# Performance work log

Measured on AMD Instinct MI355X. Metric: run time of the kernel, lower is better.

## Reference

```python
import jax, jax.numpy as jnp
import numpy as np

# Dims: B samples, D=2048 backbone feature dim (resnet50 fc.in_features),
B, D, G, R, K, C = 16384, 2048, 8, 6, 3, 16


def setup_inputs() -> dict:
    key = jax.random.key(0)
    k0, k1, k2, k3 = jax.random.split(key, 4)
    feats = jax.random.normal(k0, (B, D), dtype=jnp.float32)          # backbone output (dropout=eval identity)
    roi_ids = jax.random.randint(k1, (B,), 0, G)                       # per-sample routing id (roi_names)
    W_reg = jax.random.normal(k2, (G, R, D), dtype=jnp.float32) * 0.02  # reg_heads[roi].weight
    b_reg = jnp.zeros((G, R), dtype=jnp.float32)                       # reg_heads[roi].bias
    W_cls = jax.random.normal(k3, (G, K, C, D), dtype=jnp.float32) * 0.02  # cls_heads[roi][k].weight
    b_cls = jnp.zeros((G, K, C), dtype=jnp.float32)                    # cls_heads[roi][k].bias
    return {"feats": feats, "roi_ids": roi_ids, "W_reg": W_reg, "b_reg": b_reg,
            "W_cls": W_cls, "b_cls": b_cls}


def reference(feats, roi_ids, W_reg, b_reg, W_cls, b_cls):
    # Original loop applies, per sample i, the Linear heads of roi_names[i].
    # Vectorized: compute all-ROI head outputs densely, then gather the routed one.
    # (Same math per sample; dropout is identity in eval mode.)
    reg_all = jnp.einsum('bd,grd->bgr', feats, W_reg) + b_reg[None]        # [B, G, R]
    cls_all = jnp.einsum('bd,gkcd->bgkc', feats, W_cls) + b_cls[None]      # [B, G, K, C]
    reg = jnp.take_along_axis(reg_all, roi_ids[:, None, None], axis=1)[:, 0]            # [B, R]
    cls = jnp.take_along_axis(cls_all, roi_ids[:, None, None, None], axis=1)[:, 0]      # [B, K, C]
    return reg, cls
```

## Files before the change

### kernel.cpp

```cpp
#include <hip/hip_runtime.h>
#include <hip/hip_bf16.h>

#define NB   16384
#define NG   8
#define ND   2048
#define NR   6
#define NKC  48
#define NOUT 54
#define NT32 (NB / 32 + NG)
#define LROW 136
#define BM   32
#define KC   128
#define NCH  (ND / KC)
#define MAXT (NB / BM + NG)

typedef __attribute__((ext_vector_type(8))) short short8_t;
typedef __attribute__((ext_vector_type(4))) float f32x4;

__device__ __forceinline__ unsigned short f2bf(float x) {
    union { float f; unsigned u; } v; v.f = x;
    unsigned r = v.u + 0x7FFFu + ((v.u >> 16) & 1u);
    return (unsigned short)(r >> 16);
}

__device__ __forceinline__ short8_t cvt8(float4 a, float4 b) {
    short8_t s;
    s[0] = (short)f2bf(a.x); s[1] = (short)f2bf(a.y);
    s[2] = (short)f2bf(a.z); s[3] = (short)f2bf(a.w);
    s[4] = (short)f2bf(b.x); s[5] = (short)f2bf(b.y);
    s[6] = (short)f2bf(b.z); s[7] = (short)f2bf(b.w);
    return s;
}

__device__ __forceinline__ void gl_lds16(const void* g, void* s) {
    __builtin_amdgcn_global_load_lds(
        (const __attribute__((address_space(1))) void*)g,
        (__attribute__((address_space(3))) void*)s,
        16, 0, 0);
}

#define WAITV(N) do { asm volatile("s_waitcnt vmcnt(" #N ")" ::: "memory"); \
                      __builtin_amdgcn_sched_barrier(0); } while (0)
#define BAR() do { __builtin_amdgcn_s_barrier(); \
                   __builtin_amdgcn_sched_barrier(0); } while (0)

__global__ void hist_kernel(const int* __restrict__ roi, int* __restrict__ counts) {
    int i = blockIdx.x * 256 + threadIdx.x;
    int g = roi[i];
    int lane = threadIdx.x & 63;
    #pragma unroll
    for (int gg = 0; gg < NG; ++gg) {
        unsigned long long m = __ballot(g == gg);
        if (m && lane == (int)(__ffsll((unsigned long long)m) - 1))
            atomicAdd(&counts[gg], (int)__popcll(m));
    }
}

__global__ void scatter_kernel(const int* __restrict__ roi, const int* __restrict__ counts,
                               int* __restrict__ ranks, int* __restrict__ perm) {
    int off[NG];
    int acc = 0;
    #pragma unroll
    for (int gg = 0; gg < NG; ++gg) { off[gg] = acc; acc += counts[gg]; }
    int i = blockIdx.x * 256 + threadIdx.x;
    int g = roi[i];
    int lane = threadIdx.x & 63;
    #pragma unroll
    for (int gg = 0; gg < NG; ++gg) {
        unsigned long long m = __ballot(g == gg);
        if (!m) continue;
        int leader = (int)(__ffsll((unsigned long long)m) - 1);
        int base = 0;
        if (lane == leader) base = atomicAdd(&ranks[gg], (int)__popcll(m));
        base = __shfl(base, leader);
        if (g == gg) {
            int rank = (int)__popcll(m & ((1ull << lane) - 1ull));
            perm[off[gg] + base + rank] = i;
        }
    }
}

__global__ void prep_kernel(const int* __restrict__ roi, int* __restrict__ cnt,
                            int* __restrict__ rank,
                            const float* __restrict__ Wreg, const float* __restrict__ Wcls,
                            short* __restrict__ Wbf) {
    if (blockIdx.x < 64) {
        int i = blockIdx.x * 256 + threadIdx.x;
        int g = roi[i];
        int lane = threadIdx.x & 63;
        #pragma unroll
        for (int gg = 0; gg < NG; ++gg) {
            unsigned long long m = __ballot(g == gg);
            if (!m) continue;
            int leader = (int)(__ffsll((unsigned long long)m) - 1);
            int base = 0;
            if (lane == leader) base = atomicAdd(&cnt[gg], (int)__popcll(m));
            base = __shfl(base, leader);
            if (g == gg) {
                int r = (int)__popcll(m & ((1ull << lane) - 1ull));
                rank[i] = base + r;
            }
        }
    } else {
        int u = (blockIdx.x - 64) * 256 + threadIdx.x;
        int l = u & 63;
        int q = (u >> 6) & 7;
        int c = (u >> 9) & 31;
        int g = u >> 14;
        int n = q >> 1, ks = q & 1;
        int row = n * 16 + (l & 15);
        int k   = c * 64 + ks * 32 + (l >> 4) * 8;
        short8_t v = {0, 0, 0, 0, 0, 0, 0, 0};
        if (row < NOUT) {
            const float* s = (row < NR) ? Wreg + (size_t)(g * NR + row) * ND + k
                                        : Wcls + (size_t)(g * NKC + row - NR) * ND + k;
            float4 a = *(const float4*)s;
            float4 b = *(const float4*)(s + 4);
            v = cvt8(a, b);
        }
        *(short8_t*)(Wbf + (size_t)u * 8) = v;
    }
}

__global__ void castgather_kernel(const float* __restrict__ feats,
                                  const int* __restrict__ roi,
                                  const int* __restrict__ cnt, const int* __restrict__ rank,
                                  short* __restrict__ gathered, int* __restrict__ permp) {
    int b = blockIdx.x;
    int tid = threadIdx.x;
    int g = roi[b];
    int pre = 0;
    #pragma unroll
    for (int gg = 0; gg < NG; ++gg) if (gg < g) pre += cnt[gg];
    int pos = pre + rank[b];
    if (tid == 0) permp[pos] = b;
    const float* src = feats + (size_t)b * ND + tid * 8;
    float4 a0 = *(const float4*)(src);
    float4 a1 = *(const float4*)(src + 4);
    *(short8_t*)(gathered + (size_t)pos * ND + tid * 8) = cvt8(a0, a1);
}

__launch_bounds__(256, 4)
__global__ void gemm_s_kernel(const short* __restrict__ gathered,
                              const short* __restrict__ Wbf,
                              const float* __restrict__ breg, const float* __restrict__ bcls,
                              const int* __restrict__ cnt, const int* __restrict__ permp,
                              float* __restrict__ out) {
    __shared__ __align__(16) char lds[3][12288];

    int tid = threadIdx.x, w = tid >> 6, l = tid & 63, lr = l & 15, lq = l >> 4;
    int mt = w >> 1, nh = w & 1;

    int ts[NG + 1]; ts[0] = 0;
    int pre[NG]; int acc_ = 0;
    #pragma unroll
    for (int gg = 0; gg < NG; ++gg) {
        pre[gg] = acc_;
        acc_ += cnt[gg];
        ts[gg + 1] = ts[gg] + ((cnt[gg] + 31) >> 5);
    }
    int b = blockIdx.x;
    if (b >= ts[NG]) return;
    int g = 0;
    #pragma unroll
    for (int gg = 0; gg < NG; ++gg) if (b >= ts[gg + 1]) g = gg + 1;
    int rbase = (b - ts[g]) * 32;
    int nv = cnt[g] - rbase; if (nv > 32) nv = 32;
    int t32 = pre[g] + rbase;

    int rr = w * 8 + (l >> 3);
    const char* aSrc = (const char*)gathered + ((size_t)t32 + rr) * 4096
                     + (((l & 7) ^ (rr & 7)) << 4);
    const char* bSrc = (const char*)Wbf + (size_t)g * 262144 + 2 * w * 1024 + l * 16;

    const int ra0 = (mt * 16 + lr) * 128 + ((((0 * 4) + lq) ^ (lr & 7)) << 4);
    const int ra1 = (mt * 16 + lr) * 128 + ((((1 * 4) + lq) ^ (lr & 7)) << 4);
    const int rb00 = 4096 + ((nh * 2 + 0) * 2 + 0) * 1024 + l * 16;
    const int rb01 = 4096 + ((nh * 2 + 0) * 2 + 1) * 1024 + l * 16;
    const int rb10 = 4096 + ((nh * 2 + 1) * 2 + 0) * 1024 + l * 16;
    const int rb11 = 4096 + ((nh * 2 + 1) * 2 + 1) * 1024 + l * 16;

#define STAGE(cc, sl) do {                                                     \
        gl_lds16(aSrc + (size_t)(cc) * 128, &lds[sl][w * 1024 + l * 16]);      \
        const char* b_ = bSrc + (size_t)(cc) * 8192;                           \
        gl_lds16(b_,        &lds[sl][4096 + 2 * w * 1024 + l * 16]);           \
        gl_lds16(b_ + 1024, &lds[sl][4096 + 2 * w * 1024 + 1024 + l * 16]);    \
    } while (0)

    f32x4 acc0 = {0, 0, 0, 0}, acc1 = {0, 0, 0, 0};

    STAGE(0, 0); STAGE(1, 1);
    int csl = 0;
    #pragma unroll
    for (int c = 0; c < 32; ++c) {
        if (c + 2 < 32) STAGE(c + 2, (c + 2) % 3);
        if (c < 30)       WAITV(6);
        else if (c == 30) WAITV(3);
        else              WAITV(0);
        BAR();
        {
            const char* s = &lds[csl][0];
            short8_t af0 = *(const short8_t*)(s + ra0);
            short8_t b00 = *(const short8_t*)(s + rb00);
            short8_t b10 = *(const short8_t*)(s + rb10);
            acc0 = __builtin_amdgcn_mfma_f32_16x16x32_bf16(af0, b00, acc0, 0, 0, 0);
            acc1 = __builtin_amdgcn_mfma_f32_16x16x32_bf16(af0, b10, acc1, 0, 0, 0);
            short8_t af1 = *(const short8_t*)(s + ra1);
            short8_t b01 = *(const short8_t*)(s + rb01);
            short8_t b11 = *(const short8_t*)(s + rb11);
            acc0 = __builtin_amdgcn_mfma_f32_16x16x32_bf16(af1, b01, acc0, 0, 0, 0);
            acc1 = __builtin_amdgcn_mfma_f32_16x16x32_bf16(af1, b11, acc1, 0, 0, 0);
        }
        BAR();
        csl = (csl == 2) ? 0 : csl + 1;
    }
#undef STAGE

    const int B6 = NB * NR;
    #pragma unroll
    for (int cn = 0; cn < 2; ++cn) {
        f32x4 v = cn ? acc1 : acc0;
        int col = nh * 32 + cn * 16 + lr;
        if (col < NOUT) {
            float bias = (col < NR) ? breg[g * NR + col] : bcls[g * NKC + (col - NR)];
            #pragma unroll
            for (int j = 0; j < 4; ++j) {
                int row = mt * 16 + lq * 4 + j;
                if (row < nv) {
                    int smp = permp[t32 + row];
                    if (col < NR) out[smp * NR + col] = v[j] + bias;
                    else          out[B6 + smp * NKC + (col - NR)] = v[j] + bias;
                }
            }
        }
    }
}

__launch_bounds__(256, 3)
__global__ void gemm_kernel(const float* __restrict__ feats,
                            const float* __restrict__ Wreg, const float* __restrict__ breg,
                            const float* __restrict__ Wcls, const float* __restrict__ bcls,
                            const int* __restrict__ counts, const int* __restrict__ perm,
                            float* __restrict__ out, int stride) {
    __shared__ __align__(16) short Bsh[2][64][LROW];
    __shared__ int sRow[BM];

    int ts[NG + 1]; ts[0] = 0;
    int off[NG]; int acc = 0;
    #pragma unroll
    for (int gg = 0; gg < NG; ++gg) {
        int c = counts[gg];
        off[gg] = stride ? gg * stride : acc;
        acc += c;
        ts[gg + 1] = ts[gg] + (c + BM - 1) / BM;
    }
    int b = blockIdx.x;
    if (b >= ts[NG]) return;
    int g = 0;
    #pragma unroll
    for (int gg = 0; gg < NG; ++gg) if (b >= ts[gg + 1]) g = gg + 1;
    int gcnt  = counts[g];
    int goff  = off[g];
    int rbase = (b - ts[g]) * BM;
    int nvalid = gcnt - rbase; if (nvalid > BM) nvalid = BM;

    int tid = threadIdx.x;
    if (tid < BM) {
        int r = rbase + tid;
        if (r >= gcnt) r = gcnt - 1;
        sRow[tid] = perm[goff + r];
    }
    __syncthreads();

    int rB = tid >> 2;
    int cq = tid & 3;
    const float* wsrc = nullptr;
    if (rB < NR)        wsrc = Wreg + ((size_t)g * NR + rB) * ND + cq * 32;
    else if (rB < NOUT) wsrc = Wcls + ((size_t)g * NKC + (rB - NR)) * ND + cq * 32;

    int w = tid >> 6, l = tid & 63, lr = l & 15, lq = l >> 4;
    int mt = w & 1, nh = w >> 1;
    const float* aptr = feats + (size_t)sRow[mt * 16 + lr] * ND + lq * 8;
    const short* brp = (const short*)&Bsh[0][0][0] + (nh * 32 + lr) * LROW + lq * 8;

    f32x4 acc0 = {0, 0, 0, 0}, acc1 = {0, 0, 0, 0};
    float4 rb[8];

    if (wsrc) {
        #pragma unroll
        for (int i = 0; i < 8; ++i) rb[i] = *(const float4*)(wsrc + 4 * i);
    } else {
        #pragma unroll
        for (int i = 0; i < 8; ++i) rb[i] = make_float4(0.f, 0.f, 0.f, 0.f);
    }
    {
        short* bw = &Bsh[0][rB][cq * 32];
        #pragma unroll
        for (int j = 0; j < 4; ++j) *(short8_t*)(bw + 8 * j) = cvt8(rb[2 * j], rb[2 * j + 1]);
    }
    __syncthreads();

    #pragma unroll
    for (int c = 0; c < NCH; ++c) {
        const int cur = c & 1, nxt = cur ^ 1;
        if (c + 1 < NCH && wsrc) {
            const float* s = wsrc + (c + 1) * KC;
            #pragma unroll
            for (int i = 0; i < 8; ++i) rb[i] = *(const float4*)(s + 4 * i);
        }
        const short* bp = brp + cur * (64 * LROW);
        const float* ap = aptr + c * KC;
        #pragma unroll
        for (int ks = 0; ks < 4; ++ks) {
            float4 a0 = *(const float4*)(ap + ks * 32);
            float4 a1 = *(const float4*)(ap + ks * 32 + 4);
            short8_t af = cvt8(a0, a1);
            short8_t b0 = *(const short8_t*)(bp + ks * 32);
            short8_t b1 = *(const short8_t*)(bp + 16 * LROW + ks * 32);
            acc0 = __builtin_amdgcn_mfma_f32_16x16x32_bf16(af, b0, acc0, 0, 0, 0);
            acc1 = __builtin_amdgcn_mfma_f32_16x16x32_bf16(af, b1, acc1, 0, 0, 0);
        }
        if (c + 1 < NCH && wsrc) {
            short* bw = &Bsh[nxt][rB][cq * 32];
            #pragma unroll
            for (int j = 0; j < 4; ++j) *(short8_t*)(bw + 8 * j) = cvt8(rb[2 * j], rb[2 * j + 1]);
        } else if (c + 1 < NCH) {
            short8_t z = {0,0,0,0,0,0,0,0};
            short* bw = &Bsh[nxt][rB][cq * 32];
            #pragma unroll
            for (int j = 0; j < 4; ++j) *(short8_t*)(bw + 8 * j) = z;
        }
        __syncthreads();
    }

    const int B6 = NB * NR;
    #pragma unroll
    for (int n = 0; n < 2; ++n) {
        f32x4 v = n ? acc1 : acc0;
        int col = nh * 32 + n * 16 + lr;
        if (col < NOUT) {
            #pragma unroll
            for (int j = 0; j < 4; ++j) {
                int row = mt * 16 + lq * 4 + j;
                if (row < nvalid) {
                    int smp = sRow[row];
                    if (col < NR) out[smp * NR + col] = v[j] + breg[g * NR + col];
                    else          out[B6 + smp * NKC + (col - NR)] = v[j] + bcls[g * NKC + (col - NR)];
                }
            }
        }
    }
}

__global__ void fallback_kernel(const float* __restrict__ feats, const int* __restrict__ roi,
                                const float* __restrict__ Wreg, const float* __restrict__ breg,
                                const float* __restrict__ Wcls, const float* __restrict__ bcls,
                                float* __restrict__ out) {
    int i = blockIdx.x;
    int lane = threadIdx.x;
    int g = roi[i];
    const float* frow = feats + (size_t)i * ND;
    float f[32];
    #pragma unroll
    for (int q = 0; q < 32; ++q) f[q] = frow[lane + 64 * q];
    for (int o = 0; o < NOUT; ++o) {
        const float* wrow = (o < NR) ? Wreg + ((size_t)g * NR + o) * ND
                                     : Wcls + ((size_t)g * NKC + (o - NR)) * ND;
        float p = 0.f;
        #pragma unroll
        for (int q = 0; q < 32; ++q) p += f[q] * wrow[lane + 64 * q];
        #pragma unroll
        for (int s = 32; s; s >>= 1) p += __shfl_xor(p, s);
        if (lane == 0) {
            if (o < NR) out[i * NR + o] = p + breg[g * NR + o];
            else        out[NB * NR + i * NKC + (o - NR)] = p + bcls[g * NKC + (o - NR)];
        }
    }
}

extern "C" void kernel_launch(void* const* d_in, const int* in_sizes, int n_in,
                              void* d_out, int out_size, void* d_ws, size_t ws_size,
                              hipStream_t stream) {
    const float* feats = (const float*)d_in[0];
    const int*   roi   = (const int*)d_in[1];
    const float* Wreg  = (const float*)d_in[2];
    const float* breg  = (const float*)d_in[3];
    const float* Wcls  = (const float*)d_in[4];
    const float* bcls  = (const float*)d_in[5];
    float* out = (float*)d_out;

    const size_t wbfBytes = (size_t)NG * 131072 * 2;
    const size_t cntOff   = 2u * 1024 * 1024;
    const size_t rankOff  = cntOff + 256;
    const size_t permOff  = rankOff + (size_t)NB * 4;
    const size_t gathOff  = 4u * 1024 * 1024;
    const size_t need_t1  = gathOff + (size_t)(NB + 32) * 4096;
    const size_t need_t3  = 256 + (size_t)NB * 4;

    if (ws_size >= need_t1) {
        short* Wbf     = (short*)d_ws;
        int*   cnt     = (int*)((char*)d_ws + cntOff);
        int*   rank    = (int*)((char*)d_ws + rankOff);
        int*   permp   = (int*)((char*)d_ws + permOff);
        short* gathered= (short*)((char*)d_ws + gathOff);
        hipMemsetAsync(cnt, 0, 64, stream);
        prep_kernel<<<576, 256, 0, stream>>>(roi, cnt, rank, Wreg, Wcls, Wbf);
        castgather_kernel<<<NB, 256, 0, stream>>>(feats, roi, cnt, rank, gathered, permp);
        gemm_s_kernel<<<NT32, 256, 0, stream>>>(gathered, Wbf, breg, bcls, cnt, permp, out);
    } else if (ws_size >= need_t3) {
        int* counts = (int*)d_ws;
        int* ranks  = counts + 8;
        int* perm   = counts + 64;
        hipMemsetAsync(counts, 0, 16 * sizeof(int), stream);
        hist_kernel<<<NB / 256, 256, 0, stream>>>(roi, counts);
        scatter_kernel<<<NB / 256, 256, 0, stream>>>(roi, counts, ranks, perm);
        gemm_kernel<<<MAXT, 256, 0, stream>>>(feats, Wreg, breg, Wcls, bcls, counts, perm, out, 0);
    } else {
        fallback_kernel<<<NB, 64, 0, stream>>>(feats, roi, Wreg, breg, Wcls, bcls, out);
    }
}
```

Baseline: 84.53 us.

## Use 128-row tiles with split-K across two blocks and atomic accumulation

The grouped GEMM now uses 512-thread blocks handling 128 rows each, with each wave computing a 32x32 output sub-tile so that loaded W tiles are reused across more rows. The K dimension is split in half across paired blocks, which combine their partial results into the output through atomicAdd, with only the first half adding the bias. This requires zeroing the output with a memset beforehand and adds atomic traffic. Padding per group grows to 128 rows, so some blocks do wasted work on small groups.

```diff
diff --git a/kernel.cpp b/kernel.cpp
--- a/kernel.cpp
+++ b/kernel.cpp
@@ -7,7 +7,6 @@
 #define NR   6
 #define NKC  48
 #define NOUT 54
-#define NT32 (NB / 32 + NG)
 #define LROW 136
 #define BM   32
 #define KC   128
@@ -140,16 +139,16 @@
     *(short8_t*)(gathered + (size_t)pos * ND + tid * 8) = cvt8(a0, a1);
 }
 
-__launch_bounds__(256, 4)
-__global__ void gemm_s_kernel(const short* __restrict__ gathered,
+__launch_bounds__(512, 2)
+__global__ void gemm_w_kernel(const short* __restrict__ gathered,
                               const short* __restrict__ Wbf,
                               const float* __restrict__ breg, const float* __restrict__ bcls,
                               const int* __restrict__ cnt, const int* __restrict__ permp,
                               float* __restrict__ out) {
-    __shared__ __align__(16) char lds[3][12288];
+    __shared__ __align__(16) char lds[3][24576];
 
     int tid = threadIdx.x, w = tid >> 6, l = tid & 63, lr = l & 15, lq = l >> 4;
-    int mt = w >> 1, nh = w & 1;
+    int rw = w >> 1, ch = w & 1;
 
     int ts[NG + 1]; ts[0] = 0;
     int pre[NG]; int acc_ = 0;
@@ -157,59 +156,73 @@
     for (int gg = 0; gg < NG; ++gg) {
         pre[gg] = acc_;
         acc_ += cnt[gg];
-        ts[gg + 1] = ts[gg] + ((cnt[gg] + 31) >> 5);
+        ts[gg + 1] = ts[gg] + ((cnt[gg] + 127) >> 7);
     }
     int b = blockIdx.x;
-    if (b >= ts[NG]) return;
+    if (b >= 2 * ts[NG]) return;
+    int t = b >> 1, kh = b & 1;
     int g = 0;
     #pragma unroll
-    for (int gg = 0; gg < NG; ++gg) if (b >= ts[gg + 1]) g = gg + 1;
-    int rbase = (b - ts[g]) * 32;
-    int nv = cnt[g] - rbase; if (nv > 32) nv = 32;
-    int t32 = pre[g] + rbase;
-
-    int rr = w * 8 + (l >> 3);
-    const char* aSrc = (const char*)gathered + ((size_t)t32 + rr) * 4096
-                     + (((l & 7) ^ (rr & 7)) << 4);
-    const char* bSrc = (const char*)Wbf + (size_t)g * 262144 + 2 * w * 1024 + l * 16;
-
-    const int ra0 = (mt * 16 + lr) * 128 + ((((0 * 4) + lq) ^ (lr & 7)) << 4);
-    const int ra1 = (mt * 16 + lr) * 128 + ((((1 * 4) + lq) ^ (lr & 7)) << 4);
-    const int rb00 = 4096 + ((nh * 2 + 0) * 2 + 0) * 1024 + l * 16;
-    const int rb01 = 4096 + ((nh * 2 + 0) * 2 + 1) * 1024 + l * 16;
-    const int rb10 = 4096 + ((nh * 2 + 1) * 2 + 0) * 1024 + l * 16;
-    const int rb11 = 4096 + ((nh * 2 + 1) * 2 + 1) * 1024 + l * 16;
+    for (int gg = 0; gg < NG; ++gg) if (t >= ts[gg + 1]) g = gg + 1;
+    int rbase = (t - ts[g]) * 128;
+    int nv = cnt[g] - rbase; if (nv > 128) nv = 128;
+    int t128 = pre[g] + rbase;
+
+    int r0 = 16 * w + (l >> 3);
+    int r1 = r0 + 8;
+    const char* a0c = (const char*)gathered + ((size_t)t128 + r0) * 4096 + kh * 2048
+                    + (((l & 7) ^ (r0 & 7)) << 4);
+    const char* a1c = (const char*)gathered + ((size_t)t128 + r1) * 4096 + kh * 2048
+                    + (((l & 7) ^ (r1 & 7)) << 4);
+    const char* bSrc = (const char*)Wbf + ((size_t)(g * 32 + kh * 16) * 8 + w) * 1024 + l * 16;
 
 #define STAGE(cc, sl) do {                                                     \
-        gl_lds16(aSrc + (size_t)(cc) * 128, &lds[sl][w * 1024 + l * 16]);      \
-        const char* b_ = bSrc + (size_t)(cc) * 8192;                           \
-        gl_lds16(b_,        &lds[sl][4096 + 2 * w * 1024 + l * 16]);           \
-        gl_lds16(b_ + 1024, &lds[sl][4096 + 2 * w * 1024 + 1024 + l * 16]);    \
+        gl_lds16(a0c + (size_t)(cc) * 128, &lds[sl][(16 * w) * 128]);          \
+        gl_lds16(a1c + (size_t)(cc) * 128, &lds[sl][(16 * w + 8) * 128]);      \
+        gl_lds16(bSrc + (size_t)(cc) * 8192, &lds[sl][16384 + w * 1024]);      \
     } while (0)
 
-    f32x4 acc0 = {0, 0, 0, 0}, acc1 = {0, 0, 0, 0};
+    const int key = lr & 7;
+    const int Rb0 = (rw * 32 + lr) * 128;
+    const int Rb1 = (rw * 32 + 16 + lr) * 128;
+    const int ra00 = Rb0 + (((0 * 4 + lq) ^ key) << 4);
+    const int ra01 = Rb0 + (((1 * 4 + lq) ^ key) << 4);
+    const int ra10 = Rb1 + (((0 * 4 + lq) ^ key) << 4);
+    const int ra11 = Rb1 + (((1 * 4 + lq) ^ key) << 4);
+    const int rb00 = 16384 + ((ch * 2 + 0) * 2 + 0) * 1024 + l * 16;
+    const int rb01 = 16384 + ((ch * 2 + 0) * 2 + 1) * 1024 + l * 16;
+    const int rb10 = 16384 + ((ch * 2 + 1) * 2 + 0) * 1024 + l * 16;
+    const int rb11 = 16384 + ((ch * 2 + 1) * 2 + 1) * 1024 + l * 16;
+
+    f32x4 acc00 = {0,0,0,0}, acc01 = {0,0,0,0}, acc10 = {0,0,0,0}, acc11 = {0,0,0,0};
 
     STAGE(0, 0); STAGE(1, 1);
     int csl = 0;
     #pragma unroll
-    for (int c = 0; c < 32; ++c) {
-        if (c + 2 < 32) STAGE(c + 2, (c + 2) % 3);
-        if (c < 30)       WAITV(6);
-        else if (c == 30) WAITV(3);
+    for (int c = 0; c < 16; ++c) {
+        if (c + 2 < 16) STAGE(c + 2, (c + 2) % 3);
+        if (c < 14)       WAITV(6);
+        else if (c == 14) WAITV(3);
         else              WAITV(0);
         BAR();
         {
             const char* s = &lds[csl][0];
-            short8_t af0 = *(const short8_t*)(s + ra0);
-            short8_t b00 = *(const short8_t*)(s + rb00);
-            short8_t b10 = *(const short8_t*)(s + rb10);
-            acc0 = __builtin_amdgcn_mfma_f32_16x16x32_bf16(af0, b00, acc0, 0, 0, 0);
-            acc1 = __builtin_amdgcn_mfma_f32_16x16x32_bf16(af0, b10, acc1, 0, 0, 0);
-            short8_t af1 = *(const short8_t*)(s + ra1);
-            short8_t b01 = *(const short8_t*)(s + rb01);
-            short8_t b11 = *(const short8_t*)(s + rb11);
-            acc0 = __builtin_amdgcn_mfma_f32_16x16x32_bf16(af1, b01, acc0, 0, 0, 0);
-            acc1 = __builtin_amdgcn_mfma_f32_16x16x32_bf16(af1, b11, acc1, 0, 0, 0);
+            short8_t af00 = *(const short8_t*)(s + ra00);
+            short8_t af10 = *(const short8_t*)(s + ra10);
+            short8_t b00  = *(const short8_t*)(s + rb00);
+            short8_t b10  = *(const short8_t*)(s + rb10);
+            acc00 = __builtin_amdgcn_mfma_f32_16x16x32_bf16(af00, b00, acc00, 0, 0, 0);
+            acc01 = __builtin_amdgcn_mfma_f32_16x16x32_bf16(af00, b10, acc01, 0, 0, 0);
+            acc10 = __builtin_amdgcn_mfma_f32_16x16x32_bf16(af10, b00, acc10, 0, 0, 0);
+            acc11 = __builtin_amdgcn_mfma_f32_16x16x32_bf16(af10, b10, acc11, 0, 0, 0);
+            short8_t af01 = *(const short8_t*)(s + ra01);
+            short8_t af11 = *(const short8_t*)(s + ra11);
+            short8_t b01  = *(const short8_t*)(s + rb01);
+            short8_t b11  = *(const short8_t*)(s + rb11);
+            acc00 = __builtin_amdgcn_mfma_f32_16x16x32_bf16(af01, b01, acc00, 0, 0, 0);
+            acc01 = __builtin_amdgcn_mfma_f32_16x16x32_bf16(af01, b11, acc01, 0, 0, 0);
+            acc10 = __builtin_amdgcn_mfma_f32_16x16x32_bf16(af11, b01, acc10, 0, 0, 0);
+            acc11 = __builtin_amdgcn_mfma_f32_16x16x32_bf16(af11, b11, acc11, 0, 0, 0);
         }
         BAR();
         csl = (csl == 2) ? 0 : csl + 1;
@@ -218,18 +231,22 @@
 
     const int B6 = NB * NR;
     #pragma unroll
-    for (int cn = 0; cn < 2; ++cn) {
-        f32x4 v = cn ? acc1 : acc0;
-        int col = nh * 32 + cn * 16 + lr;
-        if (col < NOUT) {
-            float bias = (col < NR) ? breg[g * NR + col] : bcls[g * NKC + (col - NR)];
-            #pragma unroll
-            for (int j = 0; j < 4; ++j) {
-                int row = mt * 16 + lq * 4 + j;
-                if (row < nv) {
-                    int smp = permp[t32 + row];
-                    if (col < NR) out[smp * NR + col] = v[j] + bias;
-                    else          out[B6 + smp * NKC + (col - NR)] = v[j] + bias;
+    for (int mt = 0; mt < 2; ++mt) {
+        #pragma unroll
+        for (int cn = 0; cn < 2; ++cn) {
+            f32x4 v = (mt == 0) ? (cn == 0 ? acc00 : acc01) : (cn == 0 ? acc10 : acc11);
+            int col = ch * 32 + cn * 16 + lr;
+            if (col < NOUT) {
+                float bias = 0.f;
+                if (kh == 0) bias = (col < NR) ? breg[g * NR + col] : bcls[g * NKC + (col - NR)];
+                #pragma unroll
+                for (int j = 0; j < 4; ++j) {
+                    int row = rw * 32 + mt * 16 + lq * 4 + j;
+                    if (row < nv) {
+                        int smp = permp[t128 + row];
+                        if (col < NR) atomicAdd(&out[smp * NR + col], v[j] + bias);
+                        else          atomicAdd(&out[B6 + smp * NKC + (col - NR)], v[j] + bias);
+                    }
                 }
             }
         }
@@ -389,24 +406,24 @@
     const float* bcls  = (const float*)d_in[5];
     float* out = (float*)d_out;
 
-    const size_t wbfBytes = (size_t)NG * 131072 * 2;
-    const size_t cntOff   = 2u * 1024 * 1024;
-    const size_t rankOff  = cntOff + 256;
-    const size_t permOff  = rankOff + (size_t)NB * 4;
-    const size_t gathOff  = 4u * 1024 * 1024;
-    const size_t need_t1  = gathOff + (size_t)(NB + 32) * 4096;
-    const size_t need_t3  = 256 + (size_t)NB * 4;
+    const size_t cntOff  = 2u * 1024 * 1024;
+    const size_t rankOff = cntOff + 256;
+    const size_t permOff = rankOff + (size_t)NB * 4;
+    const size_t gathOff = 4u * 1024 * 1024;
+    const size_t need_t1 = gathOff + (size_t)(NB + 128) * 4096;
+    const size_t need_t3 = 256 + (size_t)NB * 4;
 
     if (ws_size >= need_t1) {
-        short* Wbf     = (short*)d_ws;
-        int*   cnt     = (int*)((char*)d_ws + cntOff);
-        int*   rank    = (int*)((char*)d_ws + rankOff);
-        int*   permp   = (int*)((char*)d_ws + permOff);
-        short* gathered= (short*)((char*)d_ws + gathOff);
+        short* Wbf      = (short*)d_ws;
+        int*   cnt      = (int*)((char*)d_ws + cntOff);
+        int*   rank     = (int*)((char*)d_ws + rankOff);
+        int*   permp    = (int*)((char*)d_ws + permOff);
+        short* gathered = (short*)((char*)d_ws + gathOff);
+        hipMemsetAsync(out, 0, (size_t)out_size * sizeof(float), stream);
         hipMemsetAsync(cnt, 0, 64, stream);
         prep_kernel<<<576, 256, 0, stream>>>(roi, cnt, rank, Wreg, Wcls, Wbf);
         castgather_kernel<<<NB, 256, 0, stream>>>(feats, roi, cnt, rank, gathered, permp);
-        gemm_s_kernel<<<NT32, 256, 0, stream>>>(gathered, Wbf, breg, bcls, cnt, permp, out);
+        gemm_w_kernel<<<272, 512, 0, stream>>>(gathered, Wbf, breg, bcls, cnt, permp, out);
     } else if (ws_size >= need_t3) {
         int* counts = (int*)d_ws;
         int* ranks  = counts + 8;
```

Result: slower. 95.84 us (+13.4%).
